# Performance work log

Measured on AMD Instinct MI355X. Metric: run time of the kernel, lower is better.

The kernel has to match this reference:

```python
import jax, jax.numpy as jnp
import numpy as np

MASK_VALUE = -1000000.0


def setup_inputs() -> dict:
    key = jax.random.key(0)
    k1, k2, k3, k4 = jax.random.split(key, 4)
    B, Lq, Lk, d = 32, 1024, 1024, 128
    return {
        "query": jax.random.normal(k1, (B, Lq, d), dtype=jnp.float32),
        "key": jax.random.normal(k2, (B, Lk, d), dtype=jnp.float32),
        "value": jax.random.normal(k3, (B, Lk, d), dtype=jnp.float32),
        "valid_length": jax.random.randint(k4, (B,), 0, Lk, dtype=jnp.int64),
    }


def reference(query, key, value, valid_length):
    # query [B, Lq, d], key/value [B, Lk, d], valid_length [B]
    d = query.shape[-1]
    # scores [B, Lq, Lk]
    scores = jnp.einsum("bqd,bkd->bqk", query, key) / jnp.sqrt(jnp.float32(d))
    Lk = key.shape[1]
    # mask positions >= valid_length with -1e6 (per-batch, broadcast over Lq)
    pos = jnp.arange(Lk)  # [Lk]
    mask = pos[None, None, :] >= valid_length[:, None, None]  # [B, 1, Lk]
    scores = jnp.where(mask, MASK_VALUE, scores)
    attn = jax.nn.softmax(scores, axis=-1)
    # dropout p=0.0 in eval -> identity
    return jnp.einsum("bqk,bkd->bqd", attn, value)
```

## Files before the change

kernel.cpp:

```cpp
#include <hip/hip_runtime.h>

#define B_N 32
#define LQ  1024
#define LK  1024
#define DH  128

typedef __attribute__((ext_vector_type(4))) float    f32x4;
typedef __attribute__((ext_vector_type(8))) short    s16x8;
typedef __attribute__((ext_vector_type(4))) _Float16 f16x4;
typedef __attribute__((ext_vector_type(8))) _Float16 f16x8;

__device__ inline unsigned short f2bf(float f) {
    union { float f; unsigned u; } c; c.f = f;
    unsigned u = c.u;
    u += 0x7fffu + ((u >> 16) & 1u);
    return (unsigned short)(u >> 16);
}

#define ESCALE 0.12751743f

__global__ __launch_bounds__(256)
void prep_kv(const float* __restrict__ K, const float* __restrict__ V,
             const int* __restrict__ VL,
             unsigned short* __restrict__ Kb, _Float16* __restrict__ Vt)
{
    __shared__ float tl[32 * 132];
    const int tid  = threadIdx.x;
    const int lane = tid & 63;
    const int wv   = tid >> 6;
    const int n    = lane & 15;
    const int quad = lane >> 4;

    const bool isK = blockIdx.x < 1024;
    const int  t   = isK ? blockIdx.x : (blockIdx.x - 1024);
    const int  b   = t >> 5, kt = t & 31;

    const int vl = VL[b];
    if (isK) {
        if (vl <= 0 || kt >= 2 * ((vl + 63) >> 6)) return;
    } else {
        const int nch = (vl > 0) ? ((vl + 63) >> 6) : 16;
        if (kt >= 2 * nch) return;
    }

    const float4* src = (const float4*)((isK ? K : V) + ((size_t)b * LK + kt * 32) * DH);
    #pragma unroll
    for (int h = 0; h < 4; ++h) {
        const int idx = h * 256 + tid;
        const int row = idx >> 5, c4 = idx & 31;
        *(float4*)&tl[row * 132 + c4 * 4] = src[idx];
    }
    __syncthreads();

    if (isK) {
        union { s16x8 v; unsigned short u[8]; } t8;
        #pragma unroll
        for (int h = 0; h < 2; ++h) {
            const int f = wv * 2 + h;
            const int tt2 = f >> 2, s = f & 3;
            const float* p = &tl[(tt2 * 16 + n) * 132 + s * 32 + quad * 8];
            const float4 a = *(const float4*)p;
            const float4 c = *(const float4*)(p + 4);
            t8.u[0] = f2bf(a.x); t8.u[1] = f2bf(a.y); t8.u[2] = f2bf(a.z); t8.u[3] = f2bf(a.w);
            t8.u[4] = f2bf(c.x); t8.u[5] = f2bf(c.y); t8.u[6] = f2bf(c.z); t8.u[7] = f2bf(c.w);
            const int w = b * 256 + (kt * 2 + tt2) * 4 + s;
            *(s16x8*)(Kb + (size_t)w * 512 + lane * 8) = t8.v;
        }
    } else {
        #pragma unroll
        for (int h = 0; h < 2; ++h) {
            const int f  = wv * 2 + h;
            const int kg = f >> 2, dp = f & 3;
            f16x8 t8;
            #pragma unroll
            for (int i = 0; i < 4; ++i) {
                const float* row = &tl[(kg * 16 + quad * 4 + i) * 132 + dp * 32 + n];
                t8[i]     = (_Float16)row[0];
                t8[4 + i] = (_Float16)row[16];
            }
            const int v = (b * 64 + kt * 2 + kg) * 4 + dp;
            *(f16x8*)(Vt + (size_t)v * 512 + lane * 8) = t8;
        }
    }
}

__global__ __launch_bounds__(128)
__attribute__((amdgpu_waves_per_eu(2, 2)))
void attn_fwd(const float* __restrict__ Q, const unsigned short* __restrict__ Kb,
              const _Float16* __restrict__ Vt, const int* __restrict__ VL,
              float* __restrict__ O)
{
    __shared__ f32x4 Om[2][8][64];
    __shared__ float Lm[2][64];

    const int tid  = threadIdx.x;
    const int lane = tid & 63;
    const int wv   = tid >> 6;
    const int quad = lane >> 4;
    const int m16  = lane & 15;

    const int idx = blockIdx.x;
    const int qg  = idx >> 5;
    const int b   = (idx & 7) | ((((idx >> 3) + (idx >> 8)) & 3) << 3);
    const int q0  = qg * 32;

    const int vl = VL[b];
    const int nch = (vl > 0) ? ((vl + 63) >> 6) : 16;
    const float emaskval = (vl == 0) ? 1.0f : 0.0f;

    s16x8 qf[2][4];
    #pragma unroll
    for (int h = 0; h < 2; ++h) {
        const float* qrow = Q + ((size_t)b * LQ + q0 + h * 16 + m16) * DH + quad * 8;
        #pragma unroll
        for (int s = 0; s < 4; ++s) {
            const float4 a = *(const float4*)(qrow + s * 32);
            const float4 c = *(const float4*)(qrow + s * 32 + 4);
            union { s16x8 v; unsigned short u[8]; } t;
            t.u[0] = f2bf(a.x); t.u[1] = f2bf(a.y); t.u[2] = f2bf(a.z); t.u[3] = f2bf(a.w);
            t.u[4] = f2bf(c.x); t.u[5] = f2bf(c.y); t.u[6] = f2bf(c.z); t.u[7] = f2bf(c.w);
            qf[h][s] = t.v;
        }
    }

    f32x4 o[2][8];
    #pragma unroll
    for (int h = 0; h < 2; ++h)
        #pragma unroll
        for (int dt = 0; dt < 8; ++dt) o[h][dt] = (f32x4){0.f, 0.f, 0.f, 0.f};
    float lrun[2] = {0.f, 0.f};

    const unsigned short* kbase = Kb + (size_t)b * (256 * 512) + lane * 8;
    const _Float16*       vbase = Vt + (size_t)b * (256 * 512) + lane * 8;

    for (int kb = wv; kb < nch; kb += 2) {
        const bool maskc = (kb * 64 + 64 > vl);
        f16x4 pA[2][4];

        #pragma unroll
        for (int g = 0; g < 4; ++g) {
            const unsigned short* kc = kbase + (size_t)((kb * 4 + g) * 4) * 512;
            f32x4 st0 = (f32x4){0.f, 0.f, 0.f, 0.f};
            f32x4 st1 = (f32x4){0.f, 0.f, 0.f, 0.f};
            #pragma unroll
            for (int s = 0; s < 4; ++s) {
                const s16x8 kf = *(const s16x8*)(kc + s * 512);
                st0 = __builtin_amdgcn_mfma_f32_16x16x32_bf16(kf, qf[0][s], st0, 0, 0, 0);
                st1 = __builtin_amdgcn_mfma_f32_16x16x32_bf16(kf, qf[1][s], st1, 0, 0, 0);
            }
            #pragma unroll
            for (int i = 0; i < 4; ++i) {
                float e0 = __builtin_amdgcn_exp2f(st0[i] * ESCALE);
                float e1 = __builtin_amdgcn_exp2f(st1[i] * ESCALE);
                if (maskc && (kb * 64 + g * 16 + quad * 4 + i >= vl)) { e0 = emaskval; e1 = emaskval; }
                lrun[0] += e0; lrun[1] += e1;
                pA[0][g][i] = (_Float16)e0;
                pA[1][g][i] = (_Float16)e1;
            }
        }

        #pragma unroll
        for (int g = 0; g < 4; ++g) {
            const _Float16* vc = vbase + (size_t)((kb * 4 + g) * 4) * 512;
            #pragma unroll
            for (int dp = 0; dp < 4; ++dp) {
                const f16x8 w  = *(const f16x8*)(vc + dp * 512);
                const f16x4 lo = __builtin_shufflevector(w, w, 0, 1, 2, 3);
                const f16x4 hi = __builtin_shufflevector(w, w, 4, 5, 6, 7);
                o[0][dp * 2]     = __builtin_amdgcn_mfma_f32_16x16x16f16(pA[0][g], lo, o[0][dp * 2],     0, 0, 0);
                o[0][dp * 2 + 1] = __builtin_amdgcn_mfma_f32_16x16x16f16(pA[0][g], hi, o[0][dp * 2 + 1], 0, 0, 0);
                o[1][dp * 2]     = __builtin_amdgcn_mfma_f32_16x16x16f16(pA[1][g], lo, o[1][dp * 2],     0, 0, 0);
                o[1][dp * 2 + 1] = __builtin_amdgcn_mfma_f32_16x16x16f16(pA[1][g], hi, o[1][dp * 2 + 1], 0, 0, 0);
            }
        }
    }

    f32x4 mine[8];
    float lmine;
    if (wv == 0) {
        #pragma unroll
        for (int dt = 0; dt < 8; ++dt) { Om[0][dt][lane] = o[1][dt]; mine[dt] = o[0][dt]; }
        Lm[0][lane] = lrun[1];
        lmine = lrun[0];
    } else {
        #pragma unroll
        for (int dt = 0; dt < 8; ++dt) { Om[1][dt][lane] = o[0][dt]; mine[dt] = o[1][dt]; }
        Lm[1][lane] = lrun[0];
        lmine = lrun[1];
    }
    __syncthreads();
    const int oh = 1 - wv;
    f32x4 om[8];
    #pragma unroll
    for (int dt = 0; dt < 8; ++dt) om[dt] = mine[dt] + Om[oh][dt][lane];
    float L = lmine + Lm[oh][lane];

    L += __shfl_xor(L, 16);
    L += __shfl_xor(L, 32);
    const size_t obase = ((size_t)b * LQ + q0 + wv * 16 + quad * 4) * DH + m16;
    #pragma unroll
    for (int r = 0; r < 4; ++r) {
        const float inv = 1.0f / __shfl(L, quad * 4 + r);
        #pragma unroll
        for (int dt = 0; dt < 8; ++dt)
            O[obase + (size_t)r * DH + dt * 16] = om[dt][r] * inv;
    }
}

extern "C" void kernel_launch(void* const* d_in, const int* in_sizes, int n_in,
                              void* d_out, int out_size, void* d_ws, size_t ws_size,
                              hipStream_t stream) {
    const float* Q  = (const float*)d_in[0];
    const float* K  = (const float*)d_in[1];
    const float* V  = (const float*)d_in[2];
    const int*   VL = (const int*)d_in[3];
    float* O = (float*)d_out;
    (void)in_sizes; (void)n_in; (void)out_size; (void)ws_size;

    unsigned short* Kb = (unsigned short*)d_ws;
    _Float16*       Vt = (_Float16*)(Kb + (size_t)B_N * 256 * 512);

    prep_kv<<<dim3(2048), dim3(256), 0, stream>>>(K, V, VL, Kb, Vt);
    attn_fwd<<<dim3(B_N * (LQ / 32)), dim3(128), 0, stream>>>(Q, Kb, Vt, VL, O);
}
```

Measured before the change: 117.5 us.

## Split attention work across four waves, one 16-row query half each

The attention kernel now launches 256 threads per block. Each wave owns one 16-row query half and one parity of key chunks, instead of two waves each handling both query halves. This halves per-wave accumulator and Q-fragment registers, which allows 4 waves per EU and more latency hiding. The cost is that K and V fragments are loaded by twice as many waves, since each K load now feeds only one MFMA instead of two, and the reduction becomes one-directional through shared memory.

```diff
diff --git a/kernel.cpp b/kernel.cpp
--- a/kernel.cpp
+++ b/kernel.cpp
@@ -84,8 +84,8 @@
     }
 }
 
-__global__ __launch_bounds__(128)
-__attribute__((amdgpu_waves_per_eu(2, 2)))
+__global__ __launch_bounds__(256)
+__attribute__((amdgpu_waves_per_eu(4, 4)))
 void attn_fwd(const float* __restrict__ Q, const unsigned short* __restrict__ Kb,
               const _Float16* __restrict__ Vt, const int* __restrict__ VL,
               float* __restrict__ O)
@@ -95,7 +95,9 @@
 
     const int tid  = threadIdx.x;
     const int lane = tid & 63;
-    const int wv   = tid >> 6;
+    const int w    = tid >> 6;
+    const int h    = w >> 1;
+    const int s0   = w & 1;
     const int quad = lane >> 4;
     const int m16  = lane & 15;
 
@@ -108,9 +110,8 @@
     const int nch = (vl > 0) ? ((vl + 63) >> 6) : 16;
     const float emaskval = (vl == 0) ? 1.0f : 0.0f;
 
-    s16x8 qf[2][4];
-    #pragma unroll
-    for (int h = 0; h < 2; ++h) {
+    s16x8 qf[4];
+    {
         const float* qrow = Q + ((size_t)b * LQ + q0 + h * 16 + m16) * DH + quad * 8;
         #pragma unroll
         for (int s = 0; s < 4; ++s) {
@@ -119,43 +120,37 @@
             union { s16x8 v; unsigned short u[8]; } t;
             t.u[0] = f2bf(a.x); t.u[1] = f2bf(a.y); t.u[2] = f2bf(a.z); t.u[3] = f2bf(a.w);
             t.u[4] = f2bf(c.x); t.u[5] = f2bf(c.y); t.u[6] = f2bf(c.z); t.u[7] = f2bf(c.w);
-            qf[h][s] = t.v;
-        }
-    }
-
-    f32x4 o[2][8];
+            qf[s] = t.v;
+        }
+    }
+
+    f32x4 o[8];
     #pragma unroll
-    for (int h = 0; h < 2; ++h)
-        #pragma unroll
-        for (int dt = 0; dt < 8; ++dt) o[h][dt] = (f32x4){0.f, 0.f, 0.f, 0.f};
-    float lrun[2] = {0.f, 0.f};
+    for (int dt = 0; dt < 8; ++dt) o[dt] = (f32x4){0.f, 0.f, 0.f, 0.f};
+    float lrun = 0.f;
 
     const unsigned short* kbase = Kb + (size_t)b * (256 * 512) + lane * 8;
     const _Float16*       vbase = Vt + (size_t)b * (256 * 512) + lane * 8;
 
-    for (int kb = wv; kb < nch; kb += 2) {
+    for (int kb = s0; kb < nch; kb += 2) {
         const bool maskc = (kb * 64 + 64 > vl);
-        f16x4 pA[2][4];
+        f16x4 pA[4];
 
         #pragma unroll
         for (int g = 0; g < 4; ++g) {
             const unsigned short* kc = kbase + (size_t)((kb * 4 + g) * 4) * 512;
-            f32x4 st0 = (f32x4){0.f, 0.f, 0.f, 0.f};
-            f32x4 st1 = (f32x4){0.f, 0.f, 0.f, 0.f};
+            f32x4 st = (f32x4){0.f, 0.f, 0.f, 0.f};
             #pragma unroll
             for (int s = 0; s < 4; ++s) {
                 const s16x8 kf = *(const s16x8*)(kc + s * 512);
-                st0 = __builtin_amdgcn_mfma_f32_16x16x32_bf16(kf, qf[0][s], st0, 0, 0, 0);
-                st1 = __builtin_amdgcn_mfma_f32_16x16x32_bf16(kf, qf[1][s], st1, 0, 0, 0);
+                st = __builtin_amdgcn_mfma_f32_16x16x32_bf16(kf, qf[s], st, 0, 0, 0);
             }
             #pragma unroll
             for (int i = 0; i < 4; ++i) {
-                float e0 = __builtin_amdgcn_exp2f(st0[i] * ESCALE);
-                float e1 = __builtin_amdgcn_exp2f(st1[i] * ESCALE);
-                if (maskc && (kb * 64 + g * 16 + quad * 4 + i >= vl)) { e0 = emaskval; e1 = emaskval; }
-                lrun[0] += e0; lrun[1] += e1;
-                pA[0][g][i] = (_Float16)e0;
-                pA[1][g][i] = (_Float16)e1;
+                float e = __builtin_amdgcn_exp2f(st[i] * ESCALE);
+                if (maskc && (kb * 64 + g * 16 + quad * 4 + i >= vl)) e = emaskval;
+                lrun += e;
+                pA[g][i] = (_Float16)e;
             }
         }
 
@@ -164,46 +159,37 @@
             const _Float16* vc = vbase + (size_t)((kb * 4 + g) * 4) * 512;
             #pragma unroll
             for (int dp = 0; dp < 4; ++dp) {
-                const f16x8 w  = *(const f16x8*)(vc + dp * 512);
-                const f16x4 lo = __builtin_shufflevector(w, w, 0, 1, 2, 3);
-                const f16x4 hi = __builtin_shufflevector(w, w, 4, 5, 6, 7);
-                o[0][dp * 2]     = __builtin_amdgcn_mfma_f32_16x16x16f16(pA[0][g], lo, o[0][dp * 2],     0, 0, 0);
-                o[0][dp * 2 + 1] = __builtin_amdgcn_mfma_f32_16x16x16f16(pA[0][g], hi, o[0][dp * 2 + 1], 0, 0, 0);
-                o[1][dp * 2]     = __builtin_amdgcn_mfma_f32_16x16x16f16(pA[1][g], lo, o[1][dp * 2],     0, 0, 0);
-                o[1][dp * 2 + 1] = __builtin_amdgcn_mfma_f32_16x16x16f16(pA[1][g], hi, o[1][dp * 2 + 1], 0, 0, 0);
-            }
-        }
-    }
-
-    f32x4 mine[8];
-    float lmine;
-    if (wv == 0) {
-        #pragma unroll
-        for (int dt = 0; dt < 8; ++dt) { Om[0][dt][lane] = o[1][dt]; mine[dt] = o[0][dt]; }
-        Lm[0][lane] = lrun[1];
-        lmine = lrun[0];
-    } else {
-        #pragma unroll
-        for (int dt = 0; dt < 8; ++dt) { Om[1][dt][lane] = o[0][dt]; mine[dt] = o[1][dt]; }
-        Lm[1][lane] = lrun[0];
-        lmine = lrun[1];
+                const f16x8 wv8 = *(const f16x8*)(vc + dp * 512);
+                const f16x4 lo  = __builtin_shufflevector(wv8, wv8, 0, 1, 2, 3);
+                const f16x4 hi  = __builtin_shufflevector(wv8, wv8, 4, 5, 6, 7);
+                o[dp * 2]     = __builtin_amdgcn_mfma_f32_16x16x16f16(pA[g], lo, o[dp * 2],     0, 0, 0);
+                o[dp * 2 + 1] = __builtin_amdgcn_mfma_f32_16x16x16f16(pA[g], hi, o[dp * 2 + 1], 0, 0, 0);
+            }
+        }
+    }
+
+    if (s0 == 1) {
+        #pragma unroll
+        for (int dt = 0; dt < 8; ++dt) Om[h][dt][lane] = o[dt];
+        Lm[h][lane] = lrun;
     }
     __syncthreads();
-    const int oh = 1 - wv;
-    f32x4 om[8];
-    #pragma unroll
-    for (int dt = 0; dt < 8; ++dt) om[dt] = mine[dt] + Om[oh][dt][lane];
-    float L = lmine + Lm[oh][lane];
-
-    L += __shfl_xor(L, 16);
-    L += __shfl_xor(L, 32);
-    const size_t obase = ((size_t)b * LQ + q0 + wv * 16 + quad * 4) * DH + m16;
-    #pragma unroll
-    for (int r = 0; r < 4; ++r) {
-        const float inv = 1.0f / __shfl(L, quad * 4 + r);
-        #pragma unroll
-        for (int dt = 0; dt < 8; ++dt)
-            O[obase + (size_t)r * DH + dt * 16] = om[dt][r] * inv;
+    if (s0 == 0) {
+        f32x4 om[8];
+        #pragma unroll
+        for (int dt = 0; dt < 8; ++dt) om[dt] = o[dt] + Om[h][dt][lane];
+        float L = lrun + Lm[h][lane];
+
+        L += __shfl_xor(L, 16);
+        L += __shfl_xor(L, 32);
+        const size_t obase = ((size_t)b * LQ + q0 + h * 16 + quad * 4) * DH + m16;
+        #pragma unroll
+        for (int r = 0; r < 4; ++r) {
+            const float inv = 1.0f / __shfl(L, quad * 4 + r);
+            #pragma unroll
+            for (int dt = 0; dt < 8; ++dt)
+                O[obase + (size_t)r * DH + dt * 16] = om[dt][r] * inv;
+        }
     }
 }
 
@@ -221,5 +207,5 @@
     _Float16*       Vt = (_Float16*)(Kb + (size_t)B_N * 256 * 512);
 
     prep_kv<<<dim3(2048), dim3(256), 0, stream>>>(K, V, VL, Kb, Vt);
-    attn_fwd<<<dim3(B_N * (LQ / 32)), dim3(128), 0, stream>>>(Q, Kb, Vt, VL, O);
-}
+    attn_fwd<<<dim3(B_N * (LQ / 32)), dim3(256), 0, stream>>>(Q, Kb, Vt, VL, O);
+}
```

After: 146.5 us. 24.7% more time.
